# Optimization experiments

Hardware: AMD Instinct MI355X
Metric: run time of the kernel (lower is better)

## Reference

```python
import jax, jax.numpy as jnp
import numpy as np

B, L_IN, D_MODEL, CONV_D, KSIZE = 16, 512, 384, 1536, 3
MEL_MAX = 4096
LN_EPS = 1e-5


def _conv1d_same(h, w, b):
    # h: [B, C_in, L], w: [C_out, C_in, K] -> [B, C_out, L]
    y = jax.lax.conv_general_dilated(h, w, window_strides=(1,), padding='SAME',
                                     dimension_numbers=('NCH', 'OIH', 'NCH'))
    return y + b[None, :, None]


def _layernorm(x, g, b):
    m = jnp.mean(x, -1, keepdims=True)
    v = jnp.mean((x - m) ** 2, -1, keepdims=True)
    return (x - m) * jax.lax.rsqrt(v + LN_EPS) * g + b


def _ffn(x, wa, ba, wb, bb):
    # Conv1D_FFT: conv(d_model->conv_d) ReLU conv(conv_d->d_model) ReLU
    h = jnp.transpose(x, (0, 2, 1))
    h = jax.nn.relu(_conv1d_same(h, wa, ba))
    h = jax.nn.relu(_conv1d_same(h, wb, bb))
    return jnp.transpose(h, (0, 2, 1))


def _dur_pred(x, w1, b1, w2, b2, g1, be1, w3, b3, w4, b4, g2, be2, wl, bl):
    h = _ffn(x, w1, b1, w2, b2)
    h = _layernorm(h, g1, be1)  # dropout is identity at eval
    h = _ffn(h, w3, b3, w4, b4)
    h = _layernorm(h, g2, be2)
    return (h @ wl + bl)[..., 0]  # [B, L_in], squeeze(-1)


def _length_regulate(x, dur, mel_max_len):
    # Equivalent to alignment @ x where alignment[b,t,j]=1 iff cum[b,j-1] <= t < cum[b,j],
    # padded with zeros out to mel_max_len (original pads output to mel_max_len).
    cum = jnp.cumsum(dur, axis=-1)                        # [B, L_in]
    total = cum[:, -1]                                    # [B]
    t = jnp.arange(mel_max_len, dtype=cum.dtype)          # [T]
    idx = jax.vmap(lambda c: jnp.searchsorted(c, t, side='right'))(cum)  # [B, T]
    idx = jnp.minimum(idx, x.shape[1] - 1)
    out = jnp.take_along_axis(x, idx[:, :, None], axis=1)  # [B, T, D]
    mask = (t[None, :] < total[:, None])[..., None]
    return out * mask


def setup_inputs() -> dict:
    key = jax.random.key(0)
    ks = jax.random.split(key, 8)
    def nrm(k, shape):
        return jax.random.normal(k, shape, jnp.float32) * 0.02
    return {
        'x': jax.random.normal(ks[0], (B, L_IN, D_MODEL), jnp.float32),
        'target': jax.random.randint(ks[1], (B, L_IN), 0, 8, jnp.int32),
        'mel_max_len': MEL_MAX,
        'w1': nrm(ks[2], (CONV_D, D_MODEL, KSIZE)), 'b1': jnp.zeros((CONV_D,), jnp.float32),
        'w2': nrm(ks[3], (D_MODEL, CONV_D, KSIZE)), 'b2': jnp.zeros((D_MODEL,), jnp.float32),
        'g1': jnp.ones((D_MODEL,), jnp.float32), 'be1': jnp.zeros((D_MODEL,), jnp.float32),
        'w3': nrm(ks[4], (CONV_D, D_MODEL, KSIZE)), 'b3': jnp.zeros((CONV_D,), jnp.float32),
        'w4': nrm(ks[5], (D_MODEL, CONV_D, KSIZE)), 'b4': jnp.zeros((D_MODEL,), jnp.float32),
        'g2': jnp.ones((D_MODEL,), jnp.float32), 'be2': jnp.zeros((D_MODEL,), jnp.float32),
        'wl': nrm(ks[6], (D_MODEL, 1)), 'bl': jnp.zeros((1,), jnp.float32),
    }


def reference(x, target, mel_max_len, w1, b1, w2, b2, g1, be1, w3, b3, w4, b4, g2, be2, wl, bl):
    dur_preds = _dur_pred(x, w1, b1, w2, b2, g1, be1, w3, b3, w4, b4, g2, be2, wl, bl)
    output = _length_regulate(x, target, mel_max_len)
    return (output, dur_preds)
```

## Files before the change

kernel.cpp:

```cpp
#include <hip/hip_runtime.h>
#include <hip/hip_bf16.h>
#include <cstddef>
#include <cstdint>

#define NB 16
#define LIN 512
#define DM 384
#define DC 1536
#define MELMAX 4096
#define LN_EPS 1e-5f

typedef __bf16 bf16x8 __attribute__((ext_vector_type(8)));
typedef float f32x4 __attribute__((ext_vector_type(4)));

#define GL2LDS(gp, lp)                                                                \
    __builtin_amdgcn_global_load_lds((const __attribute__((address_space(1))) void*)(gp), \
                                     (__attribute__((address_space(3))) void*)(lp), 16, 0, 0)

__device__ __forceinline__ float wred(float v) {
#pragma unroll
    for (int m = 32; m >= 1; m >>= 1) v += __shfl_xor(v, m, 64);
    return v;
}

__device__ __forceinline__ unsigned short f2bf(float f) {
    __hip_bfloat16 h = __float2bfloat16(f);
    return *reinterpret_cast<unsigned short*>(&h);
}

__device__ __forceinline__ float bf2f(unsigned short u) {
    return __uint_as_float(((unsigned)u) << 16);
}


__global__ void cumsum_kernel(const int* __restrict__ tgt, int* __restrict__ cum) {
    __shared__ int s[LIN];
    const int b = blockIdx.x, tid = threadIdx.x;
    s[tid] = tgt[b * LIN + tid];
    __syncthreads();
    for (int off = 1; off < LIN; off <<= 1) {
        int v = (tid >= off) ? s[tid - off] : 0;
        __syncthreads();
        s[tid] += v;
        __syncthreads();
    }
    cum[b * LIN + tid] = s[tid];
}


__global__ __launch_bounds__(256) void gather_kernel(const float* __restrict__ x,
                                                     const int* __restrict__ cum,
                                                     float* __restrict__ out) {
    const int wid = (blockIdx.x * 256 + threadIdx.x) >> 6;
    const int lane = threadIdx.x & 63;
    const int b = wid >> 12;
    const int t = wid & (MELMAX - 1);
    const int* c = cum + b * LIN;
    const int total = c[LIN - 1];
    float4* orow = reinterpret_cast<float4*>(out + ((size_t)b * MELMAX + t) * DM);
    if (t < total) {
        int lo = 0, hi = LIN;
        while (lo < hi) { int mid = (lo + hi) >> 1; if (c[mid] > t) hi = mid; else lo = mid + 1; }
        const int idx = lo < (LIN - 1) ? lo : (LIN - 1);
        const float4* xrow = reinterpret_cast<const float4*>(x + ((size_t)b * LIN + idx) * DM);
#pragma unroll
        for (int j = 0; j < 2; ++j) {
            const int p = lane + 64 * j;
            if (p < DM / 4) orow[p] = xrow[p];
        }
    } else {
        const float4 z = make_float4(0.f, 0.f, 0.f, 0.f);
#pragma unroll
        for (int j = 0; j < 2; ++j) {
            const int p = lane + 64 * j;
            if (p < DM / 4) orow[p] = z;
        }
    }
}


#define ZPAD_BLKS 96
#define CASTX_BLKS 3072
#define WCAST_BLKS 288

__global__ void prep_kernel(const float* __restrict__ x, unsigned short* __restrict__ xb,
                            unsigned short* __restrict__ hbig, unsigned short* __restrict__ h2b,
                            const float* __restrict__ w1, const float* __restrict__ w2,
                            const float* __restrict__ w3, const float* __restrict__ w4,
                            unsigned short* __restrict__ o1, unsigned short* __restrict__ o2,
                            unsigned short* __restrict__ o3, unsigned short* __restrict__ o4) {
    const int bid = blockIdx.x, tid = threadIdx.x;
    if (bid < ZPAD_BLKS) {
        const int buf = bid >> 5, rem = bid & 31;
        const int b = rem >> 1, row = (rem & 1) ? (LIN + 1) : 0;
        unsigned short* p = buf == 0 ? xb : (buf == 1 ? hbig : h2b);
        const int rl = buf == 1 ? DC : DM;
        unsigned short* base = p + ((size_t)b * (LIN + 2) + row) * rl;
        for (int c = tid; c < rl; c += 256) base[c] = 0;
        return;
    }
    if (bid < ZPAD_BLKS + CASTX_BLKS) {
        const int idx = (bid - ZPAD_BLKS) * 256 + tid;
        const float4 v = reinterpret_cast<const float4*>(x)[idx];
        const int e = idx * 4;
        const int b = e / (LIN * DM);
        const int rem = e - b * (LIN * DM);
        const int l = rem / DM;
        const int c = rem - l * DM;
        ushort4 o;
        o.x = f2bf(v.x); o.y = f2bf(v.y); o.z = f2bf(v.z); o.w = f2bf(v.w);
        *reinterpret_cast<ushort4*>(xb + ((size_t)b * (LIN + 2) + l + 1) * DM + c) = o;
        return;
    }
    const int j = bid - ZPAD_BLKS - CASTX_BLKS;
    const int which = j / WCAST_BLKS;
    const int idx = (j - which * WCAST_BLKS) * 256 + tid;
    const float* w = which == 0 ? w1 : which == 1 ? w2 : which == 2 ? w3 : w4;
    unsigned short* gg = which == 0 ? o1 : which == 1 ? o2 : which == 2 ? o3 : o4;
    const int CI = (which == 0 || which == 2) ? DM : DC;
    const int OCT = CI / 8;
    const int co = idx / OCT, ci0 = (idx - co * OCT) * 8;
    const float4* p4 = reinterpret_cast<const float4*>(w + (size_t)(co * CI + ci0) * 3);
    float v[24];
#pragma unroll
    for (int q = 0; q < 6; ++q) *reinterpret_cast<float4*>(&v[q * 4]) = p4[q];
    unsigned short tmp[3][8];
#pragma unroll
    for (int e = 0; e < 24; ++e) tmp[e % 3][e / 3] = f2bf(v[e]);
    unsigned short* ob = gg + (size_t)co * (3 * CI) + ci0;
#pragma unroll
    for (int t = 0; t < 3; ++t)
        *reinterpret_cast<uint4*>(ob + (size_t)t * CI) = *reinterpret_cast<const uint4*>(tmp[t]);
}


template <int CI, int CO, int BN>
__global__ __launch_bounds__(256, 2) void conv_mfma_kernel(const unsigned short* __restrict__ in,
                                                           const unsigned short* __restrict__ wg,
                                                           const float* __restrict__ bias,
                                                           unsigned short* __restrict__ out) {
    constexpr int BM = 128, BK = 32;
    constexpr int KC = CI / BK;
    constexpr int AGRP_REAL = 9;
    constexpr int AGRP = 12;
    constexpr int GPT = BN / 16;
    constexpr int BGRP = 3 * GPT;
    constexpr int NW_N = BN / 32;
    constexpr int NT = CO / BN;
    constexpr int NCONV = NB * (LIN / BM) * NT;

    __shared__ __align__(16) unsigned short As[2][AGRP * 512];
    __shared__ __align__(16) unsigned short Bs[2][BGRP * 512];

    const int tid = threadIdx.x;
    const int lane = tid & 63;
    const int wv = tid >> 6;

    const int orig = blockIdx.x;
    const int q = NCONV >> 3, xcd = orig & 7, o = orig >> 3;
    const int wgid = xcd * q + o;

    const int mg = wgid / NT;
    const int nt = wgid - mg * NT;
    const int b = mg >> 2;
    const int l0 = (mg & 3) * BM;
    const int n0 = nt * BN;

    const int wr = wv >> 1, wc = wv & 1;

    const unsigned short* inb = in + (size_t)b * (LIN + 2) * CI;

    f32x4 acc[4][NW_N];
#pragma unroll
    for (int m = 0; m < 4; ++m)
#pragma unroll
        for (int n = 0; n < NW_N; ++n) acc[m][n] = (f32x4){0.f, 0.f, 0.f, 0.f};

    const int lrow = lane >> 2;
    const int lch = lane & 3;
    const int fr = lane & 15, kg = lane >> 4;

    const unsigned short* aroot = inb + (size_t)l0 * CI + lch * 8;
    const unsigned short* broot = wg + (size_t)n0 * (3 * CI) + lch * 8;

#define STAGE(c, kb)                                                                      \
    do {                                                                                  \
        const unsigned short* abase = aroot + (kb) * BK;                                  \
        _Pragma("unroll")                                                                 \
        for (int g = wv; g < AGRP; g += 4) {                                              \
            const int sg = g < AGRP_REAL ? g : 0; \
            GL2LDS(abase + (size_t)(sg * 16 + lrow) * CI, &As[c][g * 512]);               \
        }                                                                                 \
        const unsigned short* bbase = broot + (kb) * BK;                                  \
        _Pragma("unroll")                                                                 \
        for (int g2 = wv; g2 < BGRP; g2 += 4) {                                           \
            const int t = g2 / GPT, gr = g2 - t * GPT;                                    \
            GL2LDS(bbase + (size_t)(gr * 16 + lrow) * (3 * CI) + (size_t)t * CI,          \
                   &Bs[c][g2 * 512]);                                                     \
        }                                                                                 \
    } while (0)

#define COMPUTE(c)                                                                        \
    do {                                                                                  \
        _Pragma("unroll")                                                                 \
        for (int t = 0; t < 3; ++t) {                                                     \
            bf16x8 aF[4], bF[NW_N];                                                       \
            _Pragma("unroll")                                                             \
            for (int m = 0; m < 4; ++m)                                                   \
                aF[m] = *reinterpret_cast<const bf16x8*>(                                 \
                    &As[c][(t + wr * 64 + m * 16 + fr) * BK + kg * 8]);                   \
            _Pragma("unroll")                                                             \
            for (int n = 0; n < NW_N; ++n)                                                \
                bF[n] = *reinterpret_cast<const bf16x8*>(                                 \
                    &Bs[c][(t * BN + wc * (BN / 2) + n * 16 + fr) * BK + kg * 8]);        \
            _Pragma("unroll")                                                             \
            for (int m = 0; m < 4; ++m)                                                   \
                _Pragma("unroll")                                                         \
                for (int n = 0; n < NW_N; ++n)                                            \
                    acc[m][n] =                                                           \
                        __builtin_amdgcn_mfma_f32_16x16x32_bf16(aF[m], bF[n], acc[m][n],  \
                                                                0, 0, 0);                 \
        }                                                                                 \
    } while (0)

#define WAITV                                                                             \
    do {                                                                                  \
        if constexpr (BN == 128)                                                          \
            asm volatile("s_waitcnt vmcnt(9)" ::: "memory");                              \
        else                                                                              \
            asm volatile("s_waitcnt vmcnt(6)" ::: "memory");                              \
    } while (0)

    STAGE(0, 0);
    STAGE(1, 1);
#pragma unroll 1
    for (int kb = 0; kb < KC; ++kb) {
        const int cur = kb & 1;
        WAITV;
        asm volatile("s_barrier" ::: "memory");
        COMPUTE(cur);
        asm volatile("s_waitcnt lgkmcnt(0)" ::: "memory");
        asm volatile("s_barrier" ::: "memory");
        int nk = kb + 2;
        if (nk >= KC) nk -= KC;
        STAGE(cur, nk);
    }
#undef STAGE
#undef COMPUTE
#undef WAITV

    const int fq = lane >> 4;
    float bv[NW_N];
#pragma unroll
    for (int n = 0; n < NW_N; ++n) bv[n] = bias[n0 + wc * (BN / 2) + n * 16 + fr];
    unsigned short* outb = out + (size_t)b * (LIN + 2) * CO;
#pragma unroll
    for (int m = 0; m < 4; ++m)
#pragma unroll
        for (int qy = 0; qy < 4; ++qy) {
            const int grow = l0 + wr * 64 + m * 16 + fq * 4 + qy + 1;
            unsigned short* orow = outb + (size_t)grow * CO + n0 + wc * (BN / 2) + fr;
#pragma unroll
            for (int n = 0; n < NW_N; ++n) {
                const float v = fmaxf(acc[m][n][qy] + bv[n], 0.f);
                orow[n * 16] = f2bf(v);
            }
        }
}


__global__ void ln_kernel(unsigned short* __restrict__ h, const float* __restrict__ g,
                          const float* __restrict__ be) {
    const int row = blockIdx.x, lane = threadIdx.x;
    const int b = row >> 9, l = row & (LIN - 1);
    unsigned short* hr = h + ((size_t)b * (LIN + 2) + l + 1) * DM;
    float v[6];
    float s = 0.f;
#pragma unroll
    for (int j = 0; j < 6; ++j) { v[j] = bf2f(hr[lane + 64 * j]); s += v[j]; }
    s = wred(s);
    const float mean = s * (1.f / DM);
    float vs = 0.f;
#pragma unroll
    for (int j = 0; j < 6; ++j) { const float d = v[j] - mean; vs += d * d; }
    vs = wred(vs);
    const float rstd = rsqrtf(vs * (1.f / DM) + LN_EPS);
#pragma unroll
    for (int j = 0; j < 6; ++j) {
        const int c = lane + 64 * j;
        hr[c] = f2bf((v[j] - mean) * rstd * g[c] + be[c]);
    }
}


__global__ void ln_linear_kernel(const unsigned short* __restrict__ h, const float* __restrict__ g,
                                 const float* __restrict__ be, const float* __restrict__ wl,
                                 const float* __restrict__ bl, float* __restrict__ dur) {
    const int row = blockIdx.x, lane = threadIdx.x;
    const int b = row >> 9, l = row & (LIN - 1);
    const unsigned short* hr = h + ((size_t)b * (LIN + 2) + l + 1) * DM;
    float v[6];
    float s = 0.f;
#pragma unroll
    for (int j = 0; j < 6; ++j) { v[j] = bf2f(hr[lane + 64 * j]); s += v[j]; }
    s = wred(s);
    const float mean = s * (1.f / DM);
    float vs = 0.f;
#pragma unroll
    for (int j = 0; j < 6; ++j) { const float d = v[j] - mean; vs += d * d; }
    vs = wred(vs);
    const float rstd = rsqrtf(vs * (1.f / DM) + LN_EPS);
    float dot = 0.f;
#pragma unroll
    for (int j = 0; j < 6; ++j) {
        const int c = lane + 64 * j;
        dot += ((v[j] - mean) * rstd * g[c] + be[c]) * wl[c];
    }
    dot = wred(dot);
    if (lane == 0) dur[row] = dot + bl[0];
}


extern "C" void kernel_launch(void* const* d_in, const int* in_sizes, int n_in,
                              void* d_out, int out_size, void* d_ws, size_t ws_size,
                              hipStream_t stream) {
    const float* x   = (const float*)d_in[0];
    const int*   tgt = (const int*)d_in[1];
    const float* w1  = (const float*)d_in[3];
    const float* b1  = (const float*)d_in[4];
    const float* w2  = (const float*)d_in[5];
    const float* b2  = (const float*)d_in[6];
    const float* g1  = (const float*)d_in[7];
    const float* be1 = (const float*)d_in[8];
    const float* w3  = (const float*)d_in[9];
    const float* b3  = (const float*)d_in[10];
    const float* w4  = (const float*)d_in[11];
    const float* b4  = (const float*)d_in[12];
    const float* g2  = (const float*)d_in[13];
    const float* be2 = (const float*)d_in[14];
    const float* wl  = (const float*)d_in[15];
    const float* bl  = (const float*)d_in[16];

    float* out = (float*)d_out;
    float* dur = out + (size_t)NB * MELMAX * DM;

    unsigned short* ws = (unsigned short*)d_ws;
    unsigned short* xb   = ws;
    unsigned short* hbig = xb + (size_t)NB * (LIN + 2) * DM;
    unsigned short* h2b  = hbig + (size_t)NB * (LIN + 2) * DC;
    unsigned short* wg1  = h2b + (size_t)NB * (LIN + 2) * DM;
    unsigned short* wg2  = wg1 + (size_t)DC * 3 * DM;
    unsigned short* wg3  = wg2 + (size_t)DM * 3 * DC;
    unsigned short* wg4  = wg3 + (size_t)DC * 3 * DM;
    int* cum = (int*)(wg4 + (size_t)DM * 3 * DC);

    cumsum_kernel<<<NB, LIN, 0, stream>>>(tgt, cum);
    gather_kernel<<<(NB * MELMAX) / 4, 256, 0, stream>>>(x, cum, out);

    prep_kernel<<<ZPAD_BLKS + CASTX_BLKS + 4 * WCAST_BLKS, 256, 0, stream>>>(
        x, xb, hbig, h2b, w1, w2, w3, w4, wg1, wg2, wg3, wg4);

    conv_mfma_kernel<DM, DC, 128><<<NB * (LIN / 128) * (DC / 128), 256, 0, stream>>>(xb, wg1, b1, hbig);
    conv_mfma_kernel<DC, DM, 64><<<NB * (LIN / 128) * (DM / 64), 256, 0, stream>>>(hbig, wg2, b2, h2b);
    ln_kernel<<<NB * LIN, 64, 0, stream>>>(h2b, g1, be1);
    conv_mfma_kernel<DM, DC, 128><<<NB * (LIN / 128) * (DC / 128), 256, 0, stream>>>(h2b, wg3, b3, hbig);
    conv_mfma_kernel<DC, DM, 64><<<NB * (LIN / 128) * (DM / 64), 256, 0, stream>>>(hbig, wg4, b4, xb);
    ln_linear_kernel<<<NB * LIN, 64, 0, stream>>>(xb, g2, be2, wl, bl, dur);
}
```

Baseline: 224.7 us.

## Add per-wave independent conv kernel for the DM->DC convolutions

Introduces a new conv kernel for the two d_model->conv_d convolutions. Each of the four waves owns a private 64x64 output tile with its own double-buffered swizzled LDS region and a 64-wide K step, so there is no block-wide barrier. The goal is to remove cross-wave synchronisation and bank conflicts and to deepen the load pipeline. In exchange, A-tile data is not shared between waves, which increases global/L2 traffic, and the 128KB LDS per block limits occupancy to one block per CU.

```diff
diff --git a/kernel.cpp b/kernel.cpp
--- a/kernel.cpp
+++ b/kernel.cpp
@@ -134,6 +134,126 @@
 }
 
 
+template <int CI, int CO>
+__global__ __launch_bounds__(256, 1) void conv_wave_kernel(const unsigned short* __restrict__ in,
+                                                           const unsigned short* __restrict__ wg,
+                                                           const float* __restrict__ bias,
+                                                           unsigned short* __restrict__ out) {
+    constexpr int K3 = 3 * CI;
+    constexpr int NKT = K3 / 64;
+    constexpr int KPT = CI / 64;
+    constexpr int NTG = CO / 256;
+    constexpr int NCONV = (NB * LIN / 64) * NTG;
+
+    __shared__ __align__(16) unsigned short smem[65536];
+
+    const int tid = threadIdx.x, lane = tid & 63, wv = tid >> 6;
+
+    const int orig = blockIdx.x;
+    const int q = NCONV >> 3, xcd = orig & 7, o = orig >> 3;
+    const int wgid = xcd * q + o;
+
+    const int mt = wgid / NTG, ng = wgid - mt * NTG;
+    const int b = mt >> 3, tm = mt & 7;
+    const int n0 = ng * 256 + wv * 64;
+
+    const unsigned short* aTile = in + ((size_t)b * (LIN + 2) + (size_t)tm * 64) * CI;
+    const unsigned short* bTile = wg + (size_t)n0 * K3;
+
+    const int lrow8 = lane >> 3;
+    const int lch = lane & 7;
+    const int swz = (lch ^ lrow8) * 8;
+    const int fr = lane & 15, kg = lane >> 4;
+
+    unsigned short* myA = smem + wv * 16384;
+
+    f32x4 acc[4][4];
+#pragma unroll
+    for (int m = 0; m < 4; ++m)
+#pragma unroll
+        for (int n = 0; n < 4; ++n) acc[m][n] = (f32x4){0.f, 0.f, 0.f, 0.f};
+
+#define STG(d, kt)                                                                        \
+    do {                                                                                  \
+        const int t_ = (kt) / KPT, kc_ = (kt) - t_ * KPT;                                 \
+        const unsigned short* ga = aTile + (size_t)(t_ + lrow8) * CI + kc_ * 64 + swz;    \
+        unsigned short* la = myA + (d) * 8192;                                            \
+        _Pragma("unroll")                                                                 \
+        for (int g = 0; g < 8; ++g)                                                       \
+            GL2LDS(ga + (size_t)(g * 8) * CI, la + g * 512);                              \
+        const unsigned short* gb = bTile + (size_t)lrow8 * K3 + (kt) * 64 + swz;          \
+        unsigned short* lb = la + 4096;                                                   \
+        _Pragma("unroll")                                                                 \
+        for (int g = 0; g < 8; ++g)                                                       \
+            GL2LDS(gb + (size_t)(g * 8) * K3, lb + g * 512);                              \
+    } while (0)
+
+#define CMP(d)                                                                            \
+    do {                                                                                  \
+        const unsigned short* la = myA + (d) * 8192;                                      \
+        bf16x8 aF[4][2], bF[4][2];                                                        \
+        _Pragma("unroll")                                                                 \
+        for (int m = 0; m < 4; ++m)                                                       \
+            _Pragma("unroll")                                                             \
+            for (int kh = 0; kh < 2; ++kh) {                                              \
+                const int r = m * 16 + fr;                                                \
+                aF[m][kh] = *reinterpret_cast<const bf16x8*>(                             \
+                    &la[r * 64 + (((kh * 4 + kg) ^ (r & 7)) * 8)]);                       \
+            }                                                                             \
+        _Pragma("unroll")                                                                 \
+        for (int n = 0; n < 4; ++n)                                                       \
+            _Pragma("unroll")                                                             \
+            for (int kh = 0; kh < 2; ++kh) {                                              \
+                const int r = n * 16 + fr;                                                \
+                bF[n][kh] = *reinterpret_cast<const bf16x8*>(                             \
+                    &la[4096 + r * 64 + (((kh * 4 + kg) ^ (r & 7)) * 8)]);                \
+            }                                                                             \
+        _Pragma("unroll")                                                                 \
+        for (int m = 0; m < 4; ++m)                                                       \
+            _Pragma("unroll")                                                             \
+            for (int n = 0; n < 4; ++n) {                                                 \
+                acc[m][n] = __builtin_amdgcn_mfma_f32_16x16x32_bf16(aF[m][0], bF[n][0],   \
+                                                                    acc[m][n], 0, 0, 0);  \
+                acc[m][n] = __builtin_amdgcn_mfma_f32_16x16x32_bf16(aF[m][1], bF[n][1],   \
+                                                                    acc[m][n], 0, 0, 0);  \
+            }                                                                             \
+    } while (0)
+
+    STG(0, 0);
+    STG(1, 1);
+#pragma unroll 1
+    for (int kt = 0; kt < NKT; ++kt) {
+        const int d = kt & 1;
+        asm volatile("s_waitcnt vmcnt(16)" ::: "memory");
+        CMP(d);
+        asm volatile("s_waitcnt lgkmcnt(0)" ::: "memory");
+        int nk = kt + 2;
+        if (nk >= NKT) nk -= NKT;
+        STG(d, nk);
+    }
+#undef STG
+#undef CMP
+    asm volatile("s_waitcnt vmcnt(0)" ::: "memory");
+
+    const int fq = lane >> 4;
+    float bv[4];
+#pragma unroll
+    for (int n = 0; n < 4; ++n) bv[n] = bias[n0 + n * 16 + fr];
+    unsigned short* outb = out + ((size_t)b * (LIN + 2) + (size_t)tm * 64 + 1) * CO;
+#pragma unroll
+    for (int m = 0; m < 4; ++m)
+#pragma unroll
+        for (int qy = 0; qy < 4; ++qy) {
+            unsigned short* orow = outb + (size_t)(m * 16 + fq * 4 + qy) * CO + n0 + fr;
+#pragma unroll
+            for (int n = 0; n < 4; ++n) {
+                const float v = fmaxf(acc[m][n][qy] + bv[n], 0.f);
+                orow[n * 16] = f2bf(v);
+            }
+        }
+}
+
+
 template <int CI, int CO, int BN>
 __global__ __launch_bounds__(256, 2) void conv_mfma_kernel(const unsigned short* __restrict__ in,
                                                            const unsigned short* __restrict__ wg,
@@ -188,7 +308,7 @@
         const unsigned short* abase = aroot + (kb) * BK;                                  \
         _Pragma("unroll")                                                                 \
         for (int g = wv; g < AGRP; g += 4) {                                              \
-            const int sg = g < AGRP_REAL ? g : 0; \
+            const int sg = g < AGRP_REAL ? g : 0;                                         \
             GL2LDS(abase + (size_t)(sg * 16 + lrow) * CI, &As[c][g * 512]);               \
         }                                                                                 \
         const unsigned short* bbase = broot + (kb) * BK;                                  \
@@ -360,10 +480,10 @@
     prep_kernel<<<ZPAD_BLKS + CASTX_BLKS + 4 * WCAST_BLKS, 256, 0, stream>>>(
         x, xb, hbig, h2b, w1, w2, w3, w4, wg1, wg2, wg3, wg4);
 
-    conv_mfma_kernel<DM, DC, 128><<<NB * (LIN / 128) * (DC / 128), 256, 0, stream>>>(xb, wg1, b1, hbig);
+    conv_wave_kernel<DM, DC><<<(NB * LIN / 64) * (DC / 256), 256, 0, stream>>>(xb, wg1, b1, hbig);
     conv_mfma_kernel<DC, DM, 64><<<NB * (LIN / 128) * (DM / 64), 256, 0, stream>>>(hbig, wg2, b2, h2b);
     ln_kernel<<<NB * LIN, 64, 0, stream>>>(h2b, g1, be1);
-    conv_mfma_kernel<DM, DC, 128><<<NB * (LIN / 128) * (DC / 128), 256, 0, stream>>>(h2b, wg3, b3, hbig);
+    conv_wave_kernel<DM, DC><<<(NB * LIN / 64) * (DC / 256), 256, 0, stream>>>(h2b, wg3, b3, hbig);
     conv_mfma_kernel<DC, DM, 64><<<NB * (LIN / 128) * (DM / 64), 256, 0, stream>>>(hbig, wg4, b4, xb);
     ln_linear_kernel<<<NB * LIN, 64, 0, stream>>>(xb, g2, be2, wl, bl, dur);
 }
```

Result: slower. 231.1 us (+2.8%).

## Triple-buffer conv MFMA K-loop and fix output tile width at 64

Applied to the files above, without the earlier changes.

Moves the implicit-GEMM conv kernel from double to triple buffering of its LDS A/B tiles, keeping two stages in flight with a vmcnt(12) wait and a manually unrolled three-phase loop. BN is now fixed at 64 for every conv, so the DM->DC convs launch twice as many narrower blocks. The goal is to hide more global-load latency and improve load balance across CUs. The cost is more LDS per block, which may lower occupancy, plus more re-reads of the A tile across N tiles. The three-phase loop relies on KC being divisible by 3, which holds for both CI=384 and CI=1536.

```diff
diff --git a/kernel.cpp b/kernel.cpp
--- a/kernel.cpp
+++ b/kernel.cpp
@@ -134,12 +134,12 @@
 }
 
 
-template <int CI, int CO, int BN>
+template <int CI, int CO>
 __global__ __launch_bounds__(256, 2) void conv_mfma_kernel(const unsigned short* __restrict__ in,
                                                            const unsigned short* __restrict__ wg,
                                                            const float* __restrict__ bias,
                                                            unsigned short* __restrict__ out) {
-    constexpr int BM = 128, BK = 32;
+    constexpr int BM = 128, BN = 64, BK = 32;
     constexpr int KC = CI / BK;
     constexpr int AGRP_REAL = 9;
     constexpr int AGRP = 12;
@@ -149,8 +149,8 @@
     constexpr int NT = CO / BN;
     constexpr int NCONV = NB * (LIN / BM) * NT;
 
-    __shared__ __align__(16) unsigned short As[2][AGRP * 512];
-    __shared__ __align__(16) unsigned short Bs[2][BGRP * 512];
+    __shared__ __align__(16) unsigned short As[3][AGRP * 512];
+    __shared__ __align__(16) unsigned short Bs[3][BGRP * 512];
 
     const int tid = threadIdx.x;
     const int lane = tid & 63;
@@ -223,31 +223,31 @@
         }                                                                                 \
     } while (0)
 
-#define WAITV                                                                             \
+#define PHASE(c, k)                                                                       \
     do {                                                                                  \
-        if constexpr (BN == 128)                                                          \
-            asm volatile("s_waitcnt vmcnt(9)" ::: "memory");                              \
-        else                                                                              \
-            asm volatile("s_waitcnt vmcnt(6)" ::: "memory");                              \
+        asm volatile("s_waitcnt vmcnt(12)" ::: "memory");  \
+        asm volatile("s_barrier" ::: "memory");             \
+        COMPUTE(c);                                                                       \
+        asm volatile("s_waitcnt lgkmcnt(0)" ::: "memory");                                \
+        asm volatile("s_barrier" ::: "memory");            \
+        int nk = (k) + 3;                                                                 \
+        if (nk >= KC) nk -= KC;                             \
+        STAGE(c, nk);                                                                     \
     } while (0)
 
     STAGE(0, 0);
     STAGE(1, 1);
+    STAGE(2, 2);
 #pragma unroll 1
-    for (int kb = 0; kb < KC; ++kb) {
-        const int cur = kb & 1;
-        WAITV;
-        asm volatile("s_barrier" ::: "memory");
-        COMPUTE(cur);
-        asm volatile("s_waitcnt lgkmcnt(0)" ::: "memory");
-        asm volatile("s_barrier" ::: "memory");
-        int nk = kb + 2;
-        if (nk >= KC) nk -= KC;
-        STAGE(cur, nk);
+    for (int kb = 0; kb < KC; kb += 3) {
+        PHASE(0, kb);
+        PHASE(1, kb + 1);
+        PHASE(2, kb + 2);
     }
 #undef STAGE
 #undef COMPUTE
-#undef WAITV
+#undef PHASE
+    asm volatile("s_waitcnt vmcnt(0)" ::: "memory");
 
     const int fq = lane >> 4;
     float bv[NW_N];
@@ -360,10 +360,10 @@
     prep_kernel<<<ZPAD_BLKS + CASTX_BLKS + 4 * WCAST_BLKS, 256, 0, stream>>>(
         x, xb, hbig, h2b, w1, w2, w3, w4, wg1, wg2, wg3, wg4);
 
-    conv_mfma_kernel<DM, DC, 128><<<NB * (LIN / 128) * (DC / 128), 256, 0, stream>>>(xb, wg1, b1, hbig);
-    conv_mfma_kernel<DC, DM, 64><<<NB * (LIN / 128) * (DM / 64), 256, 0, stream>>>(hbig, wg2, b2, h2b);
+    conv_mfma_kernel<DM, DC><<<NB * (LIN / 128) * (DC / 64), 256, 0, stream>>>(xb, wg1, b1, hbig);
+    conv_mfma_kernel<DC, DM><<<NB * (LIN / 128) * (DM / 64), 256, 0, stream>>>(hbig, wg2, b2, h2b);
     ln_kernel<<<NB * LIN, 64, 0, stream>>>(h2b, g1, be1);
-    conv_mfma_kernel<DM, DC, 128><<<NB * (LIN / 128) * (DC / 128), 256, 0, stream>>>(h2b, wg3, b3, hbig);
-    conv_mfma_kernel<DC, DM, 64><<<NB * (LIN / 128) * (DM / 64), 256, 0, stream>>>(hbig, wg4, b4, xb);
+    conv_mfma_kernel<DM, DC><<<NB * (LIN / 128) * (DC / 64), 256, 0, stream>>>(h2b, wg3, b3, hbig);
+    conv_mfma_kernel<DC, DM><<<NB * (LIN / 128) * (DM / 64), 256, 0, stream>>>(hbig, wg4, b4, xb);
     ln_linear_kernel<<<NB * LIN, 64, 0, stream>>>(xb, g2, be2, wl, bl, dur);
 }
```

Measured after the change: 226.5 us. Within noise of the previous version (+0.8%).
